# Kernel tuning notes

Measured on AMD Instinct MI355X. Metric: run time of the kernel, lower is better.

Reference implementation:

```python
import jax, jax.numpy as jnp
import numpy as np

H, DH = 8, 40            # heads, dim_head -> inner_dim = 320
SCALE = DH ** -0.5
B, N, M = 16, 4096, 77   # batch, query tokens (64x64 latent), text tokens
QD, CD, ID = 320, 768, H * DH


def setup_inputs() -> dict:
    key = jax.random.key(0)
    ks = jax.random.split(key, 7)
    x = jax.random.normal(ks[0], (B, N, QD), dtype=jnp.float32)
    context = jax.random.normal(ks[1], (B, M, CD), dtype=jnp.float32)
    # Linear weights stored as (in, out); torch nn.Linear has no bias for q/k/v
    Wq = jax.random.normal(ks[2], (QD, ID), dtype=jnp.float32) * (QD ** -0.5)
    Wk = jax.random.normal(ks[3], (CD, ID), dtype=jnp.float32) * (CD ** -0.5)
    Wv = jax.random.normal(ks[4], (CD, ID), dtype=jnp.float32) * (CD ** -0.5)
    Wo = jax.random.normal(ks[5], (ID, QD), dtype=jnp.float32) * (ID ** -0.5)
    bo = jnp.zeros((QD,), dtype=jnp.float32)
    return {"x": x, "context": context, "Wq": Wq, "Wk": Wk, "Wv": Wv, "Wo": Wo, "bo": bo}


def reference(x, context, Wq, Wk, Wv, Wo, bo):
    b, n, _ = x.shape
    m = context.shape[1]
    q = (x @ Wq).reshape(b, n, H, DH)        # to_q
    k = (context @ Wk).reshape(b, m, H, DH)  # to_k
    v = (context @ Wv).reshape(b, m, H, DH)  # to_v
    # full QK^T * scale (rank-bias path inactive: rank={} / is_add_rank=False)
    scores = jnp.einsum('bihd,bjhd->bhij', q, k) * SCALE  # [B,H,N,M]
    attn = jax.nn.softmax(scores, axis=-1)
    out = jnp.einsum('bhij,bjhd->bihd', attn, v).reshape(b, n, ID)
    return out @ Wo + bo  # to_out Linear; Dropout(p=0.0) is identity
```

## Files before the change

### kernel.cpp

```cpp
#include <hip/hip_runtime.h>

typedef unsigned short u16;
using short8 = __attribute__((ext_vector_type(8))) short;
using f32x4  = __attribute__((ext_vector_type(4))) float;

#define SCALE 0.15811388300841897f

__device__ __forceinline__ u16 f2bf(float f) {
  unsigned int u = __float_as_uint(f);
  u += 0x7fffu + ((u >> 16) & 1u);
  return (u16)(u >> 16);
}


__global__ void prep_transpose(const float* __restrict__ Wq, const float* __restrict__ Wo,
                               const float* __restrict__ Wk, const float* __restrict__ Wv,
                               u16* __restrict__ wqt, u16* __restrict__ wot,
                               u16* __restrict__ wkt, u16* __restrict__ wvt) {
  __shared__ float ld[64][65];
  const int bid = blockIdx.x;
  const float* src; u16* dst; int K; float scale; int tk, tn;
  if (bid < 25)       { src = Wq; dst = wqt; K = 320; scale = SCALE; tk = bid / 5;         tn = bid % 5; }
  else if (bid < 50)  { src = Wo; dst = wot; K = 320; scale = 1.f;   tk = (bid - 25) / 5;  tn = (bid - 25) % 5; }
  else if (bid < 110) { src = Wk; dst = wkt; K = 768; scale = 1.f;   tk = (bid - 50) / 5;  tn = (bid - 50) % 5; }
  else                { src = Wv; dst = wvt; K = 768; scale = 1.f;   tk = (bid - 110) / 5; tn = (bid - 110) % 5; }
  const int c = threadIdx.x & 63, r0 = threadIdx.x >> 6;
  for (int rr = r0; rr < 64; rr += 4)
    ld[rr][c] = src[(size_t)(tk * 64 + rr) * 320 + tn * 64 + c];
  __syncthreads();
  for (int rr = r0; rr < 64; rr += 4)
    dst[(size_t)(tn * 64 + rr) * K + tk * 64 + c] = f2bf(ld[c][rr] * scale);
}

__global__ __launch_bounds__(256, 1)
void kv_mfma(const float* __restrict__ ctx,
             const u16* __restrict__ wkt, const u16* __restrict__ wvt,
             u16* __restrict__ kbf, u16* __restrict__ vt) {
  const int b = blockIdx.x, z = blockIdx.y;
  const int tid = threadIdx.x;
  const int w = tid >> 6, l = tid & 63, l16 = l & 15, lhi = l >> 4;
  __shared__ __align__(16) u16 sctx[80][776];

  for (int i = tid; i < 80 * 192; i += 256) {
    int row = i / 192, c4 = (i - row * 192) * 4;
    ushort4 u;
    if (row < 77) {
      float4 v = *reinterpret_cast<const float4*>(&ctx[(size_t)(b * 77 + row) * 768 + c4]);
      u.x = f2bf(v.x); u.y = f2bf(v.y); u.z = f2bf(v.z); u.w = f2bf(v.w);
    } else u = (ushort4){0, 0, 0, 0};
    *reinterpret_cast<ushort4*>(&sctx[row][c4]) = u;
  }
  if (z == 0) {
    for (int i = tid; i < 8 * 80 * 3; i += 256) {
      int hm = i / 3, q = i - hm * 3;
      int h = hm / 80, m = hm - h * 80;
      *reinterpret_cast<uint4*>(&kbf[(((size_t)b * 8 + h) * 80 + m) * 64 + 40 + q * 8]) = (uint4){0, 0, 0, 0};
    }
  } else {
    for (int i = tid; i < 8 * 48 * 2; i += 256) {
      int hd = i / 2, q = i - hd * 2;
      int h = hd / 48, d = hd - h * 48;
      *reinterpret_cast<uint4*>(&vt[(((size_t)b * 8 + h) * 48 + d) * 96 + 80 + q * 8]) = (uint4){0, 0, 0, 0};
    }
    for (int i = tid; i < 8 * 8 * 10; i += 256) {
      int h = i / 80, rem = i - h * 80;
      int d = 40 + rem / 10, q = rem - (rem / 10) * 10;
      *reinterpret_cast<uint4*>(&vt[(((size_t)b * 8 + h) * 48 + d) * 96 + q * 8]) = (uint4){0, 0, 0, 0};
    }
  }
  __syncthreads();

  f32x4 acc[5][5];
  #pragma unroll
  for (int rt = 0; rt < 5; ++rt)
    #pragma unroll
    for (int nt = 0; nt < 5; ++nt) acc[rt][nt] = (f32x4){0.f, 0.f, 0.f, 0.f};

  const u16* wbase = (z == 0 ? wkt : wvt) + (size_t)(w * 80) * 768;
  #pragma unroll 2
  for (int ks = 0; ks < 24; ++ks) {
    short8 af[5];
    #pragma unroll
    for (int rt = 0; rt < 5; ++rt)
      af[rt] = *reinterpret_cast<const short8*>(&sctx[rt * 16 + l16][ks * 32 + lhi * 8]);
    short8 bf[5];
    #pragma unroll
    for (int nt = 0; nt < 5; ++nt)
      bf[nt] = *reinterpret_cast<const short8*>(&wbase[(size_t)(nt * 16 + l16) * 768 + ks * 32 + lhi * 8]);
    #pragma unroll
    for (int rt = 0; rt < 5; ++rt)
      #pragma unroll
      for (int nt = 0; nt < 5; ++nt)
        acc[rt][nt] = __builtin_amdgcn_mfma_f32_16x16x32_bf16(af[rt], bf[nt], acc[rt][nt], 0, 0, 0);
  }

  if (z == 0) {
    #pragma unroll
    for (int rt = 0; rt < 5; ++rt)
      #pragma unroll
      for (int nt = 0; nt < 5; ++nt) {
        int c = w * 80 + nt * 16 + l16, h = c / 40, d = c - h * 40;
        #pragma unroll
        for (int r = 0; r < 4; ++r) {
          int m = rt * 16 + lhi * 4 + r;
          kbf[(((size_t)b * 8 + h) * 80 + m) * 64 + d] = f2bf(m < 77 ? acc[rt][nt][r] : 0.f);
        }
      }
  } else {
    #pragma unroll
    for (int rt = 0; rt < 5; ++rt)
      #pragma unroll
      for (int nt = 0; nt < 5; ++nt) {
        int c = w * 80 + nt * 16 + l16, h = c / 40, d = c - h * 40;
        #pragma unroll
        for (int r = 0; r < 4; ++r) {
          int m = rt * 16 + lhi * 4 + r;
          vt[(((size_t)b * 8 + h) * 48 + d) * 96 + m] = f2bf(m < 77 ? acc[rt][nt][r] : 0.f);
        }
      }
  }
}

__global__ __launch_bounds__(512, 4)
void fused(const float* __restrict__ x, const u16* __restrict__ wqt,
           const u16* __restrict__ kbf, const u16* __restrict__ vtp,
           const u16* __restrict__ wot, const float* __restrict__ bo,
           float* __restrict__ out) {
  const int b  = blockIdx.y;
  const int q0 = blockIdx.x * 64;
  const int tid = threadIdx.x;
  const int w   = tid >> 6;
  const int l   = tid & 63;
  const int l16 = l & 15;
  const int lhi = l >> 4;

  __shared__ __align__(16) u16 Qx[64][344];
  __shared__ __align__(16) u16 Pt[8][16][104];

  const int ctb = (w < 4) ? 3 * w : 2 * w + 4;
  int ctv[3];
  ctv[0] = ctb;
  ctv[1] = (ctb + 1 < 19) ? ctb + 1 : 19;
  ctv[2] = (ctb + 2 < 19) ? ctb + 2 : 19;

  const float4* xin = reinterpret_cast<const float4*>(x + (size_t)(b * 4096 + q0) * 320);
  for (int i = tid; i < 64 * 80; i += 512) {
    float4 v = xin[i];
    int row = i / 80, c4 = (i - row * 80) * 4;
    ushort4 u;
    u.x = f2bf(v.x); u.y = f2bf(v.y); u.z = f2bf(v.z); u.w = f2bf(v.w);
    *reinterpret_cast<ushort4*>(&Qx[row][c4]) = u;
  }
  for (int i = tid; i < 64 * 3; i += 512) {
    int row = i / 3, q = i - row * 3;
    *reinterpret_cast<uint4*>(&Qx[row][320 + q * 8]) = (uint4){0u, 0u, 0u, 0u};
  }
  if (l < 32) {
    int r = l >> 1, q = l & 1;
    *reinterpret_cast<uint4*>(&Pt[w][r][80 + 8 * q]) = (uint4){0u, 0u, 0u, 0u};
  }
  __syncthreads();

  {
    f32x4 qacc[4][3];
    #pragma unroll
    for (int rt = 0; rt < 4; ++rt)
      #pragma unroll
      for (int nt = 0; nt < 3; ++nt) qacc[rt][nt] = (f32x4){0.f, 0.f, 0.f, 0.f};
    #pragma unroll
    for (int ks = 0; ks < 10; ++ks) {
      short8 af[4];
      #pragma unroll
      for (int rt = 0; rt < 4; ++rt)
        af[rt] = *reinterpret_cast<const short8*>(&Qx[rt * 16 + l16][ks * 32 + lhi * 8]);
      short8 bf[3];
      #pragma unroll
      for (int nt = 0; nt < 3; ++nt)
        bf[nt] = *reinterpret_cast<const short8*>(
            &wqt[(size_t)(ctv[nt] * 16 + l16) * 320 + ks * 32 + lhi * 8]);
      #pragma unroll
      for (int nt = 0; nt < 3; ++nt)
        #pragma unroll
        for (int rt = 0; rt < 4; ++rt)
          qacc[rt][nt] = __builtin_amdgcn_mfma_f32_16x16x32_bf16(af[rt], bf[nt], qacc[rt][nt], 0, 0, 0);
    }
    __syncthreads();
    #pragma unroll
    for (int nt = 0; nt < 3; ++nt) {
      int col = ctv[nt] * 16 + l16;
      #pragma unroll
      for (int rt = 0; rt < 4; ++rt)
        #pragma unroll
        for (int r = 0; r < 4; ++r)
          Qx[rt * 16 + lhi * 4 + r][col] = f2bf(qacc[rt][nt][r]);
    }
  }
  __syncthreads();

  {
    const int wq = w & 3, hg = w >> 2;
    for (int hi = 0; hi < 4; ++hi) {
      const int h = hg * 4 + hi;
      const u16* kh = kbf + (size_t)(b * 8 + h) * 80 * 64;
      const u16* vh = vtp + (size_t)(b * 8 + h) * 48 * 96;
      f32x4 sacc[5];
      #pragma unroll
      for (int mt = 0; mt < 5; ++mt) sacc[mt] = (f32x4){0.f, 0.f, 0.f, 0.f};
      #pragma unroll
      for (int ks = 0; ks < 2; ++ks) {
        short8 a = *reinterpret_cast<const short8*>(&Qx[wq * 16 + l16][h * 40 + ks * 32 + lhi * 8]);
        #pragma unroll
        for (int mt = 0; mt < 5; ++mt) {
          short8 bb = *reinterpret_cast<const short8*>(&kh[(mt * 16 + l16) * 64 + ks * 32 + lhi * 8]);
          sacc[mt] = __builtin_amdgcn_mfma_f32_16x16x32_bf16(a, bb, sacc[mt], 0, 0, 0);
        }
      }
      #pragma unroll
      for (int r = 0; r < 4; ++r) {
        float ev[5];
        float sum = 0.f;
        #pragma unroll
        for (int mt = 0; mt < 5; ++mt) {
          float s = (mt * 16 + l16 >= 77) ? -1e30f : sacc[mt][r];
          ev[mt] = __expf(s);
          sum += ev[mt];
        }
        sum += __shfl_xor(sum, 1);
        sum += __shfl_xor(sum, 2);
        sum += __shfl_xor(sum, 4);
        sum += __shfl_xor(sum, 8);
        float rs = 1.f / sum;
        int row = lhi * 4 + r;
        #pragma unroll
        for (int mt = 0; mt < 5; ++mt)
          Pt[w][row][mt * 16 + l16] = f2bf(ev[mt] * rs);
      }
      asm volatile("s_waitcnt lgkmcnt(0)" ::: "memory");
      __builtin_amdgcn_sched_barrier(0);
      f32x4 oacc[3];
      #pragma unroll
      for (int nt = 0; nt < 3; ++nt) oacc[nt] = (f32x4){0.f, 0.f, 0.f, 0.f};
      #pragma unroll
      for (int ks = 0; ks < 3; ++ks) {
        short8 a = *reinterpret_cast<const short8*>(&Pt[w][l16][ks * 32 + lhi * 8]);
        #pragma unroll
        for (int nt = 0; nt < 3; ++nt) {
          short8 bb = *reinterpret_cast<const short8*>(&vh[(nt * 16 + l16) * 96 + ks * 32 + lhi * 8]);
          oacc[nt] = __builtin_amdgcn_mfma_f32_16x16x32_bf16(a, bb, oacc[nt], 0, 0, 0);
        }
      }
      asm volatile("s_waitcnt lgkmcnt(0)" ::: "memory");
      __builtin_amdgcn_sched_barrier(0);
      #pragma unroll
      for (int nt = 0; nt < 3; ++nt) {
        int d = nt * 16 + l16;
        if (d < 40) {
          #pragma unroll
          for (int r = 0; r < 4; ++r)
            Qx[wq * 16 + lhi * 4 + r][h * 40 + d] = f2bf(oacc[nt][r]);
        }
      }
    }
  }
  __syncthreads();

  {
    const int w2 = w >> 2, w4 = w & 3;
    f32x4 cacc[2][5];
    #pragma unroll
    for (int rt = 0; rt < 2; ++rt)
      #pragma unroll
      for (int nt = 0; nt < 5; ++nt) cacc[rt][nt] = (f32x4){0.f, 0.f, 0.f, 0.f};
    #pragma unroll
    for (int ks = 0; ks < 10; ++ks) {
      short8 af[2];
      #pragma unroll
      for (int rt = 0; rt < 2; ++rt)
        af[rt] = *reinterpret_cast<const short8*>(&Qx[w2 * 32 + rt * 16 + l16][ks * 32 + lhi * 8]);
      #pragma unroll
      for (int nt = 0; nt < 5; ++nt) {
        short8 bf = *reinterpret_cast<const short8*>(
            &wot[(size_t)(w4 * 80 + nt * 16 + l16) * 320 + ks * 32 + lhi * 8]);
        #pragma unroll
        for (int rt = 0; rt < 2; ++rt)
          cacc[rt][nt] = __builtin_amdgcn_mfma_f32_16x16x32_bf16(af[rt], bf, cacc[rt][nt], 0, 0, 0);
      }
    }
    #pragma unroll
    for (int nt = 0; nt < 5; ++nt) {
      int col = w4 * 80 + nt * 16 + l16;
      float bias = bo[col];
      #pragma unroll
      for (int rt = 0; rt < 2; ++rt) {
        #pragma unroll
        for (int r = 0; r < 4; ++r) {
          int row = w2 * 32 + rt * 16 + lhi * 4 + r;
          out[(size_t)(b * 4096 + q0 + row) * 320 + col] = cacc[rt][nt][r] + bias;
        }
      }
    }
  }
}

extern "C" void kernel_launch(void* const* d_in, const int* in_sizes, int n_in,
                              void* d_out, int out_size, void* d_ws, size_t ws_size,
                              hipStream_t stream) {
  (void)in_sizes; (void)n_in; (void)out_size; (void)ws_size;
  const float* x       = (const float*)d_in[0];
  const float* context = (const float*)d_in[1];
  const float* Wq      = (const float*)d_in[2];
  const float* Wk      = (const float*)d_in[3];
  const float* Wv      = (const float*)d_in[4];
  const float* Wo      = (const float*)d_in[5];
  const float* bo      = (const float*)d_in[6];
  float* out = (float*)d_out;
  u16* ws = (u16*)d_ws;
  u16* wqt = ws;
  u16* wot = ws + 102400;
  u16* wkt = ws + 204800;
  u16* wvt = ws + 450560;
  u16* kbf = ws + 696320;
  u16* vtp = ws + 1351680;

  prep_transpose<<<170, 256, 0, stream>>>(Wq, Wo, Wk, Wv, wqt, wot, wkt, wvt);
  kv_mfma<<<dim3(16, 2), 256, 0, stream>>>(context, wkt, wvt, kbf, vtp);
  fused<<<dim3(64, 16), 512, 0, stream>>>(x, wqt, kbf, vtp, wot, bo, out);
}
```

Measured before the change: 190.3 us.

## Transpose QK^T MFMA, hoist Q fragments, prefetch V, pack P stores

Loads all four heads' Q fragments from LDS into registers once, then swaps the MFMA operands so scores come out transposed (keys along rows). This turns the softmax row-sum reduction into two cross-half shuffles instead of four, and lets P be written with packed 32-bit LDS stores. The first V fragment is prefetched before the softmax to hide global latency, and the trailing wait/sched barrier after the PV MFMAs is dropped. The cost is higher register pressure from the held Q fragments and exp values, and masking now relies on the fixed 77-key layout.

```diff
diff --git a/kernel.cpp b/kernel.cpp
--- a/kernel.cpp
+++ b/kernel.cpp
@@ -199,6 +199,14 @@
 
   {
     const int wq = w & 3, hg = w >> 2;
+    short8 qf[4][2];
+    #pragma unroll
+    for (int hi = 0; hi < 4; ++hi)
+      #pragma unroll
+      for (int ks = 0; ks < 2; ++ks)
+        qf[hi][ks] = *reinterpret_cast<const short8*>(
+            &Qx[wq * 16 + l16][(hg * 4 + hi) * 40 + ks * 32 + lhi * 8]);
+
     for (int hi = 0; hi < 4; ++hi) {
       const int h = hg * 4 + hi;
       const u16* kh = kbf + (size_t)(b * 8 + h) * 80 * 64;
@@ -208,33 +216,39 @@
       for (int mt = 0; mt < 5; ++mt) sacc[mt] = (f32x4){0.f, 0.f, 0.f, 0.f};
       #pragma unroll
       for (int ks = 0; ks < 2; ++ks) {
-        short8 a = *reinterpret_cast<const short8*>(&Qx[wq * 16 + l16][h * 40 + ks * 32 + lhi * 8]);
         #pragma unroll
         for (int mt = 0; mt < 5; ++mt) {
-          short8 bb = *reinterpret_cast<const short8*>(&kh[(mt * 16 + l16) * 64 + ks * 32 + lhi * 8]);
-          sacc[mt] = __builtin_amdgcn_mfma_f32_16x16x32_bf16(a, bb, sacc[mt], 0, 0, 0);
-        }
-      }
-      #pragma unroll
-      for (int r = 0; r < 4; ++r) {
-        float ev[5];
-        float sum = 0.f;
-        #pragma unroll
-        for (int mt = 0; mt < 5; ++mt) {
-          float s = (mt * 16 + l16 >= 77) ? -1e30f : sacc[mt][r];
-          ev[mt] = __expf(s);
-          sum += ev[mt];
-        }
-        sum += __shfl_xor(sum, 1);
-        sum += __shfl_xor(sum, 2);
-        sum += __shfl_xor(sum, 4);
-        sum += __shfl_xor(sum, 8);
-        float rs = 1.f / sum;
-        int row = lhi * 4 + r;
-        #pragma unroll
-        for (int mt = 0; mt < 5; ++mt)
-          Pt[w][row][mt * 16 + l16] = f2bf(ev[mt] * rs);
-      }
+          short8 ka = *reinterpret_cast<const short8*>(&kh[(mt * 16 + l16) * 64 + ks * 32 + lhi * 8]);
+          sacc[mt] = __builtin_amdgcn_mfma_f32_16x16x32_bf16(ka, qf[hi][ks], sacc[mt], 0, 0, 0);
+        }
+      }
+      short8 vb0[3];
+      #pragma unroll
+      for (int nt = 0; nt < 3; ++nt)
+        vb0[nt] = *reinterpret_cast<const short8*>(&vh[(nt * 16 + l16) * 96 + lhi * 8]);
+      float ev[5][4];
+      float psum = 0.f;
+      #pragma unroll
+      for (int mt = 0; mt < 5; ++mt)
+        #pragma unroll
+        for (int r = 0; r < 4; ++r) {
+          float e = __expf(sacc[mt][r]);
+          if (mt == 4 && lhi * 4 + r >= 13) e = 0.f;
+          ev[mt][r] = e;
+          psum += e;
+        }
+      psum += __shfl_xor(psum, 16);
+      psum += __shfl_xor(psum, 32);
+      float rs = 1.f / psum;
+      asm volatile("s_waitcnt lgkmcnt(0)" ::: "memory");
+      #pragma unroll
+      for (int mt = 0; mt < 5; ++mt)
+        #pragma unroll
+        for (int j = 0; j < 2; ++j) {
+          unsigned pk = (unsigned)f2bf(ev[mt][2 * j] * rs) |
+                        ((unsigned)f2bf(ev[mt][2 * j + 1] * rs) << 16);
+          *reinterpret_cast<unsigned*>(&Pt[w][l16][mt * 16 + lhi * 4 + 2 * j]) = pk;
+        }
       asm volatile("s_waitcnt lgkmcnt(0)" ::: "memory");
       __builtin_amdgcn_sched_barrier(0);
       f32x4 oacc[3];
@@ -245,12 +259,11 @@
         short8 a = *reinterpret_cast<const short8*>(&Pt[w][l16][ks * 32 + lhi * 8]);
         #pragma unroll
         for (int nt = 0; nt < 3; ++nt) {
-          short8 bb = *reinterpret_cast<const short8*>(&vh[(nt * 16 + l16) * 96 + ks * 32 + lhi * 8]);
+          short8 bb = (ks == 0) ? vb0[nt]
+                                : *reinterpret_cast<const short8*>(&vh[(nt * 16 + l16) * 96 + ks * 32 + lhi * 8]);
           oacc[nt] = __builtin_amdgcn_mfma_f32_16x16x32_bf16(a, bb, oacc[nt], 0, 0, 0);
         }
       }
-      asm volatile("s_waitcnt lgkmcnt(0)" ::: "memory");
-      __builtin_amdgcn_sched_barrier(0);
       #pragma unroll
       for (int nt = 0; nt < 3; ++nt) {
         int d = nt * 16 + l16;
```

After: 188.2 us. No clear change (-1.1%).
